# Optimization experiments

Measured on AMD Instinct MI355X. Metric: run time of the kernel, lower is better.

Reference implementation:

```python
import jax, jax.numpy as jnp
import numpy as np

B, S, HID = 1, 2048, 2048
NH = 32
NOPE, ROPE = 128, 64
QK = NOPE + ROPE
VD = 128
KV_RANK = 512
SW = 128            # sliding window (layer_types[layer_idx] == 'sliding_attention')
SCALE = QK ** -0.5
NEG = -1e9


def rotate_half(x):
    h = x.shape[-1] // 2
    return jnp.concatenate([-x[..., h:], x[..., :h]], axis=-1)


def setup_inputs() -> dict:
    key = jax.random.key(0)
    ks = jax.random.split(key, 8)

    def n(k, shape, s=0.02):
        return jax.random.normal(k, shape, dtype=jnp.float32) * s

    hidden = jax.random.normal(ks[0], (B, S, HID), dtype=jnp.float32)
    # HF-style RoPE tables, broadcast to [B, S, ROPE]
    pos = jnp.arange(S, dtype=jnp.float32)
    inv = 1.0 / (10000.0 ** (jnp.arange(0, ROPE, 2, dtype=jnp.float32) / ROPE))
    ang = pos[:, None] * inv[None, :]
    ang = jnp.concatenate([ang, ang], axis=-1)
    cos = jnp.broadcast_to(jnp.cos(ang)[None], (B, S, ROPE))
    sin = jnp.broadcast_to(jnp.sin(ang)[None], (B, S, ROPE))
    return dict(
        hidden_states=hidden, cos=cos, sin=sin,
        Wq=n(ks[1], (HID, NH * QK)), bq=jnp.zeros((NH * QK,), jnp.float32),
        Wkva=n(ks[2], (HID, KV_RANK + ROPE)), bkva=jnp.zeros((KV_RANK + ROPE,), jnp.float32),
        Wkvb=n(ks[3], (KV_RANK, NH * (NOPE + VD))),
        Wo=n(ks[4], (NH * VD, HID)), bo=jnp.zeros((HID,), jnp.float32),
        sinks=jax.random.normal(ks[5], (NH,), dtype=jnp.float32),
    )


def reference(hidden_states, cos, sin, Wq, bq, Wkva, bkva, Wkvb, Wo, bo, sinks):
    b, s = hidden_states.shape[:2]
    # Q projection -> [b, nh, s, qk_head_dim]
    q = (hidden_states @ Wq + bq).reshape(b, s, NH, QK).transpose(0, 2, 1, 3)
    q_nope, q_rope = q[..., :NOPE], q[..., NOPE:]
    # MLA: compressed KV latent + shared (MQA) rope key
    ckv = hidden_states @ Wkva + bkva                       # [b, s, rank+rope]
    kv_lat, k_rope = ckv[..., :KV_RANK], ckv[..., KV_RANK:]
    kv = (kv_lat @ Wkvb).reshape(b, s, NH, NOPE + VD).transpose(0, 2, 1, 3)
    k_nope, v = kv[..., :NOPE], kv[..., NOPE:]              # [b, nh, s, *]
    k_rope = k_rope.reshape(b, 1, s, ROPE)                  # mla_rope_num_kv_heads = 1
    # RoPE (HF apply_rotary_pos_emb, unsqueeze head dim)
    c, si = cos[:, None], sin[:, None]
    q_rope = q_rope * c + rotate_half(q_rope) * si
    k_rope = k_rope * c + rotate_half(k_rope) * si
    k_rope = jnp.broadcast_to(k_rope, (b, NH, s, ROPE))     # repeat_kv
    qs = jnp.concatenate([q_nope, q_rope], axis=-1)
    kk = jnp.concatenate([k_nope, k_rope], axis=-1)
    # attention logits with causal + sliding-window mask
    logits = jnp.einsum('bhqd,bhkd->bhqk', qs, kk) * SCALE
    i = jnp.arange(s)[:, None]
    j = jnp.arange(s)[None, :]
    allowed = (j <= i) & (i - j < SW)
    logits = jnp.where(allowed[None, None], logits, NEG)
    # sink-augmented softmax: append learned per-head sink logit, softmax, drop it
    sink = jnp.broadcast_to(sinks[None, :, None, None], (b, NH, s, 1))
    probs = jax.nn.softmax(jnp.concatenate([logits, sink], axis=-1), axis=-1)[..., :-1]
    out = jnp.einsum('bhqk,bhkd->bhqd', probs, v)           # [b, nh, s, vd]
    out = out.transpose(0, 2, 1, 3).reshape(b, s, NH * VD)
    return out @ Wo + bo
```

## Files before the change

kernel.cpp:

```cpp
#include <hip/hip_runtime.h>
#include <hip/hip_bf16.h>
#include <math.h>

#define S_LEN 2048
#define HID_DIM 2048
#define NH 32
#define NOPE 128
#define ROPE_D 64
#define QKD 192
#define VD 128
#define KV_RANK 512
#define SW 128
#define NQK (NH*QKD)
#define CKV_N (KV_RANK+ROPE_D)
#define KVN (NH*(NOPE+VD))
#define KNW (NH*NOPE)
#define OUT_HID 2048
#define ATT_SCALE 0.07216878364870323f
#define NEG_INF (-1e30f)

typedef __bf16 bf16x8 __attribute__((ext_vector_type(8)));
typedef float  f32x4  __attribute__((ext_vector_type(4)));

__device__ __forceinline__ void async_load16(const void* gp, void* lp) {
    __builtin_amdgcn_global_load_lds(
        (const __attribute__((address_space(1))) void*)gp,
        (__attribute__((address_space(3))) void*)lp, 16, 0, 0);
}

__global__ __launch_bounds__(256)
void prep(const float* __restrict__ hidden, __hip_bfloat16* __restrict__ hid_bf,
          const float* __restrict__ Wq,   __hip_bfloat16* __restrict__ WqT,
          const float* __restrict__ Wkva, __hip_bfloat16* __restrict__ WkvaT,
          const float* __restrict__ Wkvb, __hip_bfloat16* __restrict__ WkvbT,
          const float* __restrict__ Wo,   __hip_bfloat16* __restrict__ WoT)
{
    __shared__ float tile[64][65];
    int b = blockIdx.x;
    const int t = threadIdx.x;

    if (b < 4096) {
        int i = b * 256 + t;
        float4 v = ((const float4*)hidden)[i];
        hid_bf[i * 4 + 0] = __float2bfloat16(v.x);
        hid_bf[i * 4 + 1] = __float2bfloat16(v.y);
        hid_bf[i * 4 + 2] = __float2bfloat16(v.z);
        hid_bf[i * 4 + 3] = __float2bfloat16(v.w);
        return;
    }
    b -= 4096;
    const float* src; __hip_bfloat16* dst; int rows, cols, CX;
    if (b < 3072)                { src = Wq;   dst = WqT;   rows = 2048; cols = 6144; CX = 96;  }
    else if ((b -= 3072) < 288)  { src = Wkva; dst = WkvaT; rows = 2048; cols = 576;  CX = 9;   }
    else if ((b -= 288) < 1024)  { src = Wkvb; dst = WkvbT; rows = 512;  cols = 8192; CX = 128; }
    else { b -= 1024;              src = Wo;   dst = WoT;   rows = 4096; cols = 2048; CX = 32;  }

    const int bx = b % CX, by = b / CX;
    const int r0 = by * 64, c0 = bx * 64;

    {
        const int r  = t >> 4;
        const int c4 = (t & 15) * 4;
        #pragma unroll
        for (int i = 0; i < 4; ++i) {
            const int rr = r + i * 16;
            float4 v = *(const float4*)&src[(size_t)(r0 + rr) * cols + c0 + c4];
            tile[rr][c4 + 0] = v.x;
            tile[rr][c4 + 1] = v.y;
            tile[rr][c4 + 2] = v.z;
            tile[rr][c4 + 3] = v.w;
        }
    }
    __syncthreads();
    const int tx = t & 63, ty = t >> 6;
    #pragma unroll
    for (int i = 0; i < 16; ++i) {
        const int dr = ty + i * 4;
        dst[(size_t)(c0 + dr) * rows + r0 + tx] = __float2bfloat16(tile[tx][dr]);
    }
}

#define BAR()   __builtin_amdgcn_s_barrier()
#define LGKM0() asm volatile("s_waitcnt lgkmcnt(0)" ::: "memory")
#define VMC(n)  asm volatile("s_waitcnt vmcnt(" #n ")" ::: "memory")

__device__ __forceinline__ void gemm256_core(
    const __hip_bfloat16* __restrict__ A, int lda,
    const __hip_bfloat16* __restrict__ Bt, int ldbt,
    int m0, int n0, int kbeg, int nit,
    __hip_bfloat16* lds, f32x4 (&acc)[8][4])
{
    const int t = threadIdx.x;
    const int w = t >> 6, L = t & 63;
    const int lane15 = L & 15, quad = L >> 4;
    const int wr = w >> 2, wc = w & 3;

    const int prw = w * 8 + (L >> 3);
    const int c8  = ((L & 7) ^ ((L >> 3) & 7)) * 8;
    const __hip_bfloat16* gA = A  + (size_t)(m0 + prw) * lda  + kbeg + c8;
    const __hip_bfloat16* gB = Bt + (size_t)(n0 + prw) * ldbt + kbeg + c8;
    const int uA = w * 512;
    const int uB = 16384 + w * 512;

    const int cx0 = ((quad)     ^ (L & 7)) * 8;
    const int cx1 = ((4 + quad) ^ (L & 7)) * 8;
    const int ra  = wr * 8192 + lane15 * 64;
    const int rb  = 16384 + (wc >> 1) * 8192 + (wc & 1) * 4096 + lane15 * 64;

    bf16x8 af[4][2], bfr[4][2];

    auto STG_A = [&](int buf, int h, int kt) {
        const __hip_bfloat16* g = gA + (size_t)h * 128 * lda + kt * 64;
        __hip_bfloat16* lp = lds + buf * 32768 + h * 8192 + uA;
        async_load16(g, lp);
        async_load16(g + (size_t)64 * lda, lp + 4096);
    };
    auto STG_B = [&](int buf, int h, int kt) {
        const __hip_bfloat16* g = gB + (size_t)h * 128 * ldbt + kt * 64;
        __hip_bfloat16* lp = lds + buf * 32768 + h * 8192 + uB;
        async_load16(g, lp);
        async_load16(g + (size_t)64 * ldbt, lp + 4096);
    };
    auto LDA4 = [&](int buf, int mlo) {
        const __hip_bfloat16* p0 = lds + buf * 32768 + ra;
        #pragma unroll
        for (int j = 0; j < 4; ++j) {
            af[j][0] = *(const bf16x8*)(const void*)(p0 + (mlo + j) * 1024 + cx0);
            af[j][1] = *(const bf16x8*)(const void*)(p0 + (mlo + j) * 1024 + cx1);
        }
    };
    auto LDB2 = [&](int buf, int nlo) {
        const __hip_bfloat16* p0 = lds + buf * 32768 + rb;
        #pragma unroll
        for (int n = 0; n < 2; ++n) {
            bfr[nlo + n][0] = *(const bf16x8*)(const void*)(p0 + (nlo + n) * 1024 + cx0);
            bfr[nlo + n][1] = *(const bf16x8*)(const void*)(p0 + (nlo + n) * 1024 + cx1);
        }
    };
    auto MMQ = [&](int mlo, int nlo) {
        __builtin_amdgcn_s_setprio(1);
        #pragma unroll
        for (int j = 0; j < 4; ++j)
            #pragma unroll
            for (int n = 0; n < 2; ++n)
                #pragma unroll
                for (int ks = 0; ks < 2; ++ks)
                    acc[mlo + j][nlo + n] = __builtin_amdgcn_mfma_f32_16x16x32_bf16(
                        af[j][ks], bfr[nlo + n][ks], acc[mlo + j][nlo + n], 0, 0, 0);
        __builtin_amdgcn_s_setprio(0);
    };

    STG_A(0, 0, 0); STG_B(0, 0, 0); STG_B(0, 1, 0); STG_A(0, 1, 0);
    STG_A(1, 0, 1); STG_B(1, 0, 1); STG_B(1, 1, 1);
    VMC(6);
    BAR();

    for (int it = 0; it < nit; ++it) {
        const int t0 = 2 * it, t1 = t0 + 1;
        const bool nl = (it + 1 < nit);
        LDA4(0, 0); LDB2(0, 0); STG_A(1, 1, t1);
        BAR(); LGKM0(); MMQ(0, 0); BAR();
        LDB2(0, 2);
        BAR(); LGKM0(); MMQ(0, 2); BAR();
        LDA4(0, 4); if (nl) STG_B(0, 0, t0 + 2);
        BAR(); LGKM0(); MMQ(4, 2); BAR();
        if (nl) { STG_B(0, 1, t0 + 2); STG_A(0, 0, t0 + 2); }
        BAR(); MMQ(4, 0);
        if (nl) { VMC(6); } else { VMC(0); }
        BAR();
        LDA4(1, 0); LDB2(1, 0); if (nl) STG_A(0, 1, t0 + 2);
        BAR(); LGKM0(); MMQ(0, 0); BAR();
        LDB2(1, 2);
        BAR(); LGKM0(); MMQ(0, 2); BAR();
        LDA4(1, 4); if (nl) STG_B(1, 0, t1 + 2);
        BAR(); LGKM0(); MMQ(4, 2); BAR();
        if (nl) { STG_B(1, 1, t1 + 2); STG_A(1, 0, t1 + 2); }
        BAR(); MMQ(4, 0);
        if (nl) { VMC(6); }
        BAR();
    }
}

__global__ __launch_bounds__(512)
void gemm_q_ckv(const __hip_bfloat16* __restrict__ A,
                const __hip_bfloat16* __restrict__ BtQ,
                const __hip_bfloat16* __restrict__ BtKVA,
                const float* __restrict__ bq,
                const float* __restrict__ bkva,
                const float* __restrict__ cosb, const float* __restrict__ sinb,
                __hip_bfloat16* __restrict__ C,
                __hip_bfloat16* __restrict__ kvlat,
                __hip_bfloat16* __restrict__ kr)
{
    __shared__ __hip_bfloat16 lds[65536];
    const int bid = blockIdx.x;
    const bool is_q = (bid < 192);
    const int m0 = (is_q ? (bid / 24) : ((bid - 192) / 3)) * 256;
    const int n0 = (is_q ? (bid % 24) : ((bid - 192) % 3)) * 256;

    f32x4 acc[8][4];
    #pragma unroll
    for (int mi = 0; mi < 8; ++mi)
        #pragma unroll
        for (int ni = 0; ni < 4; ++ni) acc[mi][ni] = (f32x4){0.f, 0.f, 0.f, 0.f};

    gemm256_core(A, HID_DIM, is_q ? BtQ : BtKVA, HID_DIM, m0, n0, 0,
                 HID_DIM / 128, lds, acc);

    const int t = threadIdx.x;
    const int w = t >> 6, L = t & 63;
    const int lane15 = L & 15, quad = L >> 4;
    const int wr = w >> 2, wc = w & 3;
    const int ns = n0 + wc * 64;

    if (is_q) {
        const bool do_rope = ((ns % 192) == 128);
        float bv[4];
        #pragma unroll
        for (int ni = 0; ni < 4; ++ni) bv[ni] = bq[ns + ni * 16 + lane15];

        #pragma unroll
        for (int mi = 0; mi < 8; ++mi) {
            const int rbase = m0 + wr * 128 + mi * 16 + quad * 4;
            float vv[4][4];
            #pragma unroll
            for (int ni = 0; ni < 4; ++ni)
                #pragma unroll
                for (int p = 0; p < 4; ++p) vv[ni][p] = acc[mi][ni][p] + bv[ni];
            if (do_rope) {
                #pragma unroll
                for (int ni = 0; ni < 2; ++ni) {
                    const int dd = ni * 16 + lane15;
                    #pragma unroll
                    for (int p = 0; p < 4; ++p) {
                        const int srow = rbase + p;
                        const float c0 = cosb[srow * ROPE_D + dd];
                        const float c1 = cosb[srow * ROPE_D + dd + 32];
                        const float s0 = sinb[srow * ROPE_D + dd];
                        const float s1 = sinb[srow * ROPE_D + dd + 32];
                        const float x0 = vv[ni][p], x1 = vv[ni + 2][p];
                        vv[ni][p]     = x0 * c0 - x1 * s0;
                        vv[ni + 2][p] = x1 * c1 + x0 * s1;
                    }
                }
            }
            #pragma unroll
            for (int ni = 0; ni < 4; ++ni) {
                const int c = ns + ni * 16 + lane15;
                #pragma unroll
                for (int p = 0; p < 4; ++p)
                    C[(size_t)(rbase + p) * NQK + c] = __float2bfloat16(vv[ni][p] * ATT_SCALE);
            }
        }
    } else if (ns < KV_RANK) {
        float bv[4];
        #pragma unroll
        for (int ni = 0; ni < 4; ++ni) bv[ni] = bkva[ns + ni * 16 + lane15];
        #pragma unroll
        for (int mi = 0; mi < 8; ++mi) {
            const int s = m0 + wr * 128 + mi * 16 + quad * 4;
            #pragma unroll
            for (int ni = 0; ni < 4; ++ni) {
                const int c = ns + ni * 16 + lane15;
                #pragma unroll
                for (int p = 0; p < 4; ++p)
                    kvlat[(size_t)(s + p) * KV_RANK + c] =
                        __float2bfloat16(acc[mi][ni][p] + bv[ni]);
            }
        }
    } else if (ns == KV_RANK) {
        #pragma unroll
        for (int mi = 0; mi < 8; ++mi) {
            const int sb = m0 + wr * 128 + mi * 16 + quad * 4;
            #pragma unroll
            for (int ni = 0; ni < 2; ++ni) {
                const int d = ni * 16 + lane15;
                const float ba = bkva[512 + d], bb = bkva[544 + d];
                #pragma unroll
                for (int p = 0; p < 4; ++p) {
                    const int s = sb + p;
                    const float a = acc[mi][ni][p] + ba;
                    const float b = acc[mi][ni + 2][p] + bb;
                    const float c0 = cosb[s * ROPE_D + d], c1 = cosb[s * ROPE_D + d + 32];
                    const float s0 = sinb[s * ROPE_D + d], s1 = sinb[s * ROPE_D + d + 32];
                    kr[(size_t)s * ROPE_D + d]      = __float2bfloat16(a * c0 - b * s0);
                    kr[(size_t)s * ROPE_D + d + 32] = __float2bfloat16(b * c1 + a * s1);
                }
            }
        }
    }
}

__global__ __launch_bounds__(512)
void gemm_kv256(const __hip_bfloat16* __restrict__ A,
                const __hip_bfloat16* __restrict__ Bt,
                __hip_bfloat16* __restrict__ kn,
                __hip_bfloat16* __restrict__ vt)
{
    __shared__ __hip_bfloat16 lds[65536];
    const int m0 = blockIdx.y * 256, n0 = blockIdx.x * 256;
    f32x4 acc[8][4];
    #pragma unroll
    for (int mi = 0; mi < 8; ++mi)
        #pragma unroll
        for (int ni = 0; ni < 4; ++ni) acc[mi][ni] = (f32x4){0.f, 0.f, 0.f, 0.f};

    gemm256_core(A, KV_RANK, Bt, KV_RANK, m0, n0, 0, KV_RANK / 128, lds, acc);

    const int t = threadIdx.x;
    const int w = t >> 6, L = t & 63;
    const int lane15 = L & 15, quad = L >> 4;
    const int wr = w >> 2, wc = w & 3;
    const int ns = n0 + wc * 64;

    #pragma unroll
    for (int mi = 0; mi < 8; ++mi) {
        const int rbase = m0 + wr * 128 + mi * 16 + quad * 4;
        #pragma unroll
        for (int ni = 0; ni < 4; ++ni) {
            const int c = ns + ni * 16 + lane15;
            const int h = c >> 8, d = c & 255;
            if (d < NOPE) {
                #pragma unroll
                for (int p = 0; p < 4; ++p)
                    kn[(size_t)(rbase + p) * KNW + h * NOPE + d] = __float2bfloat16(acc[mi][ni][p]);
            } else {
                ushort4 pk;
                __hip_bfloat16 b0 = __float2bfloat16(acc[mi][ni][0]);
                __hip_bfloat16 b1 = __float2bfloat16(acc[mi][ni][1]);
                __hip_bfloat16 b2 = __float2bfloat16(acc[mi][ni][2]);
                __hip_bfloat16 b3 = __float2bfloat16(acc[mi][ni][3]);
                pk.x = *(unsigned short*)&b0; pk.y = *(unsigned short*)&b1;
                pk.z = *(unsigned short*)&b2; pk.w = *(unsigned short*)&b3;
                *(ushort4*)(vt + (size_t)(h * VD + (d - NOPE)) * S_LEN + rbase) = pk;
            }
        }
    }
}

__global__ __launch_bounds__(512)
void gemm_partial256(const __hip_bfloat16* __restrict__ A, int lda,
                     const __hip_bfloat16* __restrict__ Bt, int ldbt,
                     float* __restrict__ P, int ldp, size_t zstride, int KL)
{
    __shared__ __hip_bfloat16 lds[65536];
    const int m0 = blockIdx.y * 256, n0 = blockIdx.x * 256;
    const int z  = blockIdx.z;
    f32x4 acc[8][4];
    #pragma unroll
    for (int mi = 0; mi < 8; ++mi)
        #pragma unroll
        for (int ni = 0; ni < 4; ++ni) acc[mi][ni] = (f32x4){0.f, 0.f, 0.f, 0.f};

    gemm256_core(A, lda, Bt, ldbt, m0, n0, z * KL, KL / 128, lds, acc);

    const int t = threadIdx.x;
    const int w = t >> 6, L = t & 63;
    const int lane15 = L & 15, quad = L >> 4;
    const int wr = w >> 2, wc = w & 3;
    float* Pz = P + (size_t)z * zstride;

    #pragma unroll
    for (int mi = 0; mi < 8; ++mi) {
        const int rbase = m0 + wr * 128 + mi * 16 + quad * 4;
        #pragma unroll
        for (int ni = 0; ni < 4; ++ni) {
            const int c = n0 + wc * 64 + ni * 16 + lane15;
            #pragma unroll
            for (int p = 0; p < 4; ++p)
                Pz[(size_t)(rbase + p) * ldp + c] = acc[mi][ni][p];
        }
    }
}

__global__ __launch_bounds__(256)
void wo_reduce4(const float* __restrict__ P, const float* __restrict__ bo,
                float* __restrict__ out)
{
    const size_t i = (size_t)blockIdx.x * 256 + threadIdx.x;
    const size_t zs = (size_t)S_LEN * OUT_HID;
    float4 a = ((const float4*)P)[i];
    float4 b = ((const float4*)(P + zs))[i];
    float4 c = ((const float4*)(P + 2 * zs))[i];
    float4 d = ((const float4*)(P + 3 * zs))[i];
    const int col = (int)((i * 4) & (OUT_HID - 1));
    float4 bb = *(const float4*)(bo + col);
    float4 o;
    o.x = a.x + b.x + c.x + d.x + bb.x;
    o.y = a.y + b.y + c.y + d.y + bb.y;
    o.z = a.z + b.z + c.z + d.z + bb.z;
    o.w = a.w + b.w + c.w + d.w + bb.w;
    ((float4*)out)[i] = o;
}

#define SS 170
#define SP 168
#define KSTR 200
#define VSTR 40

__global__ __launch_bounds__(256)
void attn_mfma2(const __hip_bfloat16* __restrict__ q,
                const __hip_bfloat16* __restrict__ kn,
                const __hip_bfloat16* __restrict__ kr,
                const __hip_bfloat16* __restrict__ vt,
                const float* __restrict__ sinks,
                __hip_bfloat16* __restrict__ out)
{
    __shared__ float lds_s[32 * SS];
    __shared__ __hip_bfloat16 lds_p[32 * SP];
    __shared__ __hip_bfloat16 lds_kv[32 * KSTR];

    const int h  = blockIdx.y;
    const int q0 = blockIdx.x * 32;
    const int t  = threadIdx.x;
    const int w  = t >> 6;
    const int L  = t & 63;
    const int lane15 = L & 15, quad = L >> 4;
    const int wm = (w & 1) * 16;
    const int wn = (w >> 1) * 16;

    int lo = q0 - SW + 1; if (lo < 0) lo = 0;
    const int cb = lo & ~31;
    const int nc = ((q0 - cb) >> 5) + 1;

    bf16x8 qf[6];
    {
        const __hip_bfloat16* qrow = q + (size_t)(q0 + wm + lane15) * NQK + h * QKD;
        #pragma unroll
        for (int kk = 0; kk < 6; ++kk)
            qf[kk] = *(const bf16x8*)(const void*)(qrow + kk * 32 + quad * 8);
    }

    for (int cc = 0; cc < nc; ++cc) {
        const int c0 = cb + cc * 32;
        __syncthreads();
        #pragma unroll
        for (int e = t; e < 768; e += 256) {
            const int row = e / 24, slot = e % 24;
            const int j = c0 + row;
            const __hip_bfloat16* g = (slot < 16)
                ? kn + (size_t)j * KNW + h * NOPE + slot * 8
                : kr + (size_t)j * ROPE_D + (slot - 16) * 8;
            *(bf16x8*)(void*)(lds_kv + row * KSTR + slot * 8) = *(const bf16x8*)(const void*)g;
        }
        __syncthreads();

        f32x4 s = (f32x4){0.f, 0.f, 0.f, 0.f};
        #pragma unroll
        for (int kk = 0; kk < 6; ++kk) {
            bf16x8 bf = *(const bf16x8*)(const void*)(lds_kv + (wn + lane15) * KSTR + kk * 32 + quad * 8);
            s = __builtin_amdgcn_mfma_f32_16x16x32_bf16(qf[kk], bf, s, 0, 0, 0);
        }
        const int j = c0 + wn + lane15;
        #pragma unroll
        for (int p = 0; p < 4; ++p) {
            const int i = q0 + wm + quad * 4 + p;
            const bool ok = (j <= i) && (i - j < SW);
            lds_s[(wm + quad * 4 + p) * SS + cc * 32 + wn + lane15] = ok ? s[p] : NEG_INF;
        }
    }
    __syncthreads();

    {
        const int r = t >> 3, g = t & 7;
        const int ncols = nc * 32;
        const float sink = sinks[h];
        float mx = sink;
        for (int c = g; c < ncols; c += 8)
            mx = fmaxf(mx, lds_s[r * SS + c]);
        #pragma unroll
        for (int off = 1; off < 8; off <<= 1)
            mx = fmaxf(mx, __shfl_xor(mx, off));
        float sum = 0.f;
        for (int c = g; c < ncols; c += 8) {
            float e = __expf(lds_s[r * SS + c] - mx);
            lds_s[r * SS + c] = e;
            sum += e;
        }
        #pragma unroll
        for (int off = 1; off < 8; off <<= 1)
            sum += __shfl_xor(sum, off);
        const float inv = 1.0f / (sum + __expf(sink - mx));
        for (int c = g; c < ncols; c += 8)
            lds_p[r * SP + c] = __float2bfloat16(lds_s[r * SS + c] * inv);
    }

    f32x4 oacc[4];
    #pragma unroll
    for (int ni = 0; ni < 4; ++ni) oacc[ni] = (f32x4){0.f, 0.f, 0.f, 0.f};

    for (int cc = 0; cc < nc; ++cc) {
        const int c0 = cb + cc * 32;
        __syncthreads();
        #pragma unroll
        for (int e = t; e < 512; e += 256) {
            const int row = e >> 2, slot = e & 3;
            *(bf16x8*)(void*)(lds_kv + row * VSTR + slot * 8) =
                *(const bf16x8*)(const void*)(vt + (size_t)(h * VD + row) * S_LEN + c0 + slot * 8);
        }
        __syncthreads();

        bf16x8 ap = *(const bf16x8*)(const void*)(lds_p + (wm + lane15) * SP + cc * 32 + quad * 8);
        #pragma unroll
        for (int ni = 0; ni < 4; ++ni) {
            bf16x8 bv = *(const bf16x8*)(const void*)(lds_kv + ((w >> 1) * 64 + ni * 16 + lane15) * VSTR + quad * 8);
            oacc[ni] = __builtin_amdgcn_mfma_f32_16x16x32_bf16(ap, bv, oacc[ni], 0, 0, 0);
        }
    }

    #pragma unroll
    for (int ni = 0; ni < 4; ++ni) {
        const int col = h * VD + (w >> 1) * 64 + ni * 16 + lane15;
        #pragma unroll
        for (int p = 0; p < 4; ++p) {
            const int row = q0 + wm + quad * 4 + p;
            out[(size_t)row * (NH * VD) + col] = __float2bfloat16(oacc[ni][p]);
        }
    }
}

extern "C" void kernel_launch(void* const* d_in, const int* in_sizes, int n_in,
                              void* d_out, int out_size, void* d_ws, size_t ws_size,
                              hipStream_t stream) {
    const float* hidden = (const float*)d_in[0];
    const float* cosb   = (const float*)d_in[1];
    const float* sinb   = (const float*)d_in[2];
    const float* Wq     = (const float*)d_in[3];
    const float* bq     = (const float*)d_in[4];
    const float* Wkva   = (const float*)d_in[5];
    const float* bkva   = (const float*)d_in[6];
    const float* Wkvb   = (const float*)d_in[7];
    const float* Wo     = (const float*)d_in[8];
    const float* bo     = (const float*)d_in[9];
    const float* sinks  = (const float*)d_in[10];
    float* out = (float*)d_out;

    uint8_t* p = (uint8_t*)d_ws;
    __hip_bfloat16* attn_bf = (__hip_bfloat16*)p; p += (size_t)S_LEN * NH * VD * 2;
    __hip_bfloat16* WoT     = (__hip_bfloat16*)p; p += (size_t)OUT_HID * (NH*VD) * 2;
    __hip_bfloat16* q_bf    = (__hip_bfloat16*)p; p += (size_t)S_LEN * NQK * 2;
    __hip_bfloat16* hid_bf  = (__hip_bfloat16*)p; p += (size_t)S_LEN * HID_DIM * 2;
    __hip_bfloat16* WqT     = (__hip_bfloat16*)p; p += (size_t)NQK * HID_DIM * 2;
    __hip_bfloat16* WkvaT   = (__hip_bfloat16*)p; p += (size_t)640 * HID_DIM * 2;
    __hip_bfloat16* WkvbT   = (__hip_bfloat16*)p; p += (size_t)KVN * KV_RANK * 2;
    __hip_bfloat16* kn_bf   = (__hip_bfloat16*)p; p += (size_t)S_LEN * KNW * 2;
    __hip_bfloat16* vt_bf   = (__hip_bfloat16*)p; p += (size_t)S_LEN * NH * VD * 2;
    __hip_bfloat16* kr_bf   = (__hip_bfloat16*)p; p += (size_t)S_LEN * ROPE_D * 2;
    __hip_bfloat16* kvlat   = (__hip_bfloat16*)p; p += (size_t)S_LEN * KV_RANK * 2;
    float* WoP = (float*)q_bf;

    prep<<<10528, 256, 0, stream>>>(hidden, hid_bf, Wq, WqT, Wkva, WkvaT,
                                    Wkvb, WkvbT, Wo, WoT);

    gemm_q_ckv<<<216, 512, 0, stream>>>(
        hid_bf, WqT, WkvaT, bq, bkva, cosb, sinb, q_bf, kvlat, kr_bf);

    gemm_kv256<<<dim3(KVN / 256, S_LEN / 256), 512, 0, stream>>>(
        kvlat, WkvbT, kn_bf, vt_bf);

    attn_mfma2<<<dim3(S_LEN / 32, NH), 256, 0, stream>>>(
        q_bf, kn_bf, kr_bf, vt_bf, sinks, attn_bf);

    gemm_partial256<<<dim3(OUT_HID / 256, S_LEN / 256, 4), 512, 0, stream>>>(
        attn_bf, NH * VD, WoT, NH * VD, WoP, OUT_HID, (size_t)S_LEN * OUT_HID, 1024);

    wo_reduce4<<<(S_LEN * OUT_HID / 4) / 256, 256, 0, stream>>>(WoP, bo, out);
}
```

Measured before the change: 357.2 us.

## Overlap Wkvb/Wo weight transposes with Q/CKV GEMM using extra blocks

Moves the bf16 transpose of Wkvb and Wo out of the prep kernel and into 40 extra workgroups appended to the Q/CKV GEMM launch, so that conversion work fills CUs left idle by the 216 GEMM blocks on a 256-CU device. It also reorders the GEMM main loop so the vmcnt wait happens before the barrier that precedes the final MMA quarter, which merges two barrier regions. The extra blocks share the launch's large LDS and 512-thread configuration. Their grid-stride loop may extend the GEMM kernel's tail if the transposes take longer than the GEMM.

Result: slower. 376.9 us (+5.5%).

```diff
diff --git a/kernel.cpp b/kernel.cpp
--- a/kernel.cpp
+++ b/kernel.cpp
@@ -31,9 +31,7 @@
 __global__ __launch_bounds__(256)
 void prep(const float* __restrict__ hidden, __hip_bfloat16* __restrict__ hid_bf,
           const float* __restrict__ Wq,   __hip_bfloat16* __restrict__ WqT,
-          const float* __restrict__ Wkva, __hip_bfloat16* __restrict__ WkvaT,
-          const float* __restrict__ Wkvb, __hip_bfloat16* __restrict__ WkvbT,
-          const float* __restrict__ Wo,   __hip_bfloat16* __restrict__ WoT)
+          const float* __restrict__ Wkva, __hip_bfloat16* __restrict__ WkvaT)
 {
     __shared__ float tile[64][65];
     int b = blockIdx.x;
@@ -50,10 +48,8 @@
     }
     b -= 4096;
     const float* src; __hip_bfloat16* dst; int rows, cols, CX;
-    if (b < 3072)                { src = Wq;   dst = WqT;   rows = 2048; cols = 6144; CX = 96;  }
-    else if ((b -= 3072) < 288)  { src = Wkva; dst = WkvaT; rows = 2048; cols = 576;  CX = 9;   }
-    else if ((b -= 288) < 1024)  { src = Wkvb; dst = WkvbT; rows = 512;  cols = 8192; CX = 128; }
-    else { b -= 1024;              src = Wo;   dst = WoT;   rows = 4096; cols = 2048; CX = 32;  }
+    if (b < 3072) { src = Wq;   dst = WqT;   rows = 2048; cols = 6144; CX = 96; }
+    else { b -= 3072; src = Wkva; dst = WkvaT; rows = 2048; cols = 576;  CX = 9;  }
 
     const int bx = b % CX, by = b / CX;
     const int r0 = by * 64, c0 = bx * 64;
@@ -164,20 +160,17 @@
         BAR(); LGKM0(); MMQ(0, 2); BAR();
         LDA4(0, 4); if (nl) STG_B(0, 0, t0 + 2);
         BAR(); LGKM0(); MMQ(4, 2); BAR();
-        if (nl) { STG_B(0, 1, t0 + 2); STG_A(0, 0, t0 + 2); }
-        BAR(); MMQ(4, 0);
-        if (nl) { VMC(6); } else { VMC(0); }
-        BAR();
+        if (nl) { STG_B(0, 1, t0 + 2); STG_A(0, 0, t0 + 2); VMC(6); }
+        else    { VMC(0); }
+        BAR(); MMQ(4, 0); BAR();
         LDA4(1, 0); LDB2(1, 0); if (nl) STG_A(0, 1, t0 + 2);
         BAR(); LGKM0(); MMQ(0, 0); BAR();
         LDB2(1, 2);
         BAR(); LGKM0(); MMQ(0, 2); BAR();
         LDA4(1, 4); if (nl) STG_B(1, 0, t1 + 2);
         BAR(); LGKM0(); MMQ(4, 2); BAR();
-        if (nl) { STG_B(1, 1, t1 + 2); STG_A(1, 0, t1 + 2); }
-        BAR(); MMQ(4, 0);
-        if (nl) { VMC(6); }
-        BAR();
+        if (nl) { STG_B(1, 1, t1 + 2); STG_A(1, 0, t1 + 2); VMC(6); }
+        BAR(); MMQ(4, 0); BAR();
     }
 }
 
@@ -190,10 +183,45 @@
                 const float* __restrict__ cosb, const float* __restrict__ sinb,
                 __hip_bfloat16* __restrict__ C,
                 __hip_bfloat16* __restrict__ kvlat,
-                __hip_bfloat16* __restrict__ kr)
+                __hip_bfloat16* __restrict__ kr,
+                const float* __restrict__ Wkvb, __hip_bfloat16* __restrict__ WkvbT,
+                const float* __restrict__ Wo,   __hip_bfloat16* __restrict__ WoT)
 {
     __shared__ __hip_bfloat16 lds[65536];
     const int bid = blockIdx.x;
+    const int t = threadIdx.x;
+
+    if (bid >= 216) {
+        float (*tile)[65] = (float (*)[65])(void*)lds;
+        const int r  = t >> 4;
+        const int c4 = (t & 15) * 4;
+        const int tx = t & 63, ty = t >> 6;
+        for (int id = bid - 216; id < 3072; id += 40) {
+            const float* src; __hip_bfloat16* dst; int rows, cols, CX, tid;
+            if (id < 1024) { src = Wkvb; dst = WkvbT; rows = 512;  cols = 8192; CX = 128; tid = id; }
+            else           { src = Wo;   dst = WoT;   rows = 4096; cols = 2048; CX = 32;  tid = id - 1024; }
+            const int bx = tid % CX, by = tid / CX;
+            const int r0 = by * 64, c0 = bx * 64;
+            #pragma unroll
+            for (int i = 0; i < 2; ++i) {
+                const int rr = r + i * 32;
+                float4 v = *(const float4*)&src[(size_t)(r0 + rr) * cols + c0 + c4];
+                tile[rr][c4 + 0] = v.x;
+                tile[rr][c4 + 1] = v.y;
+                tile[rr][c4 + 2] = v.z;
+                tile[rr][c4 + 3] = v.w;
+            }
+            __syncthreads();
+            #pragma unroll
+            for (int i = 0; i < 8; ++i) {
+                const int dr = ty + i * 8;
+                dst[(size_t)(c0 + dr) * rows + r0 + tx] = __float2bfloat16(tile[tx][dr]);
+            }
+            __syncthreads();
+        }
+        return;
+    }
+
     const bool is_q = (bid < 192);
     const int m0 = (is_q ? (bid / 24) : ((bid - 192) / 3)) * 256;
     const int n0 = (is_q ? (bid % 24) : ((bid - 192) % 3)) * 256;
@@ -207,7 +235,6 @@
     gemm256_core(A, HID_DIM, is_q ? BtQ : BtKVA, HID_DIM, m0, n0, 0,
                  HID_DIM / 128, lds, acc);
 
-    const int t = threadIdx.x;
     const int w = t >> 6, L = t & 63;
     const int lane15 = L & 15, quad = L >> 4;
     const int wr = w >> 2, wc = w & 3;
@@ -549,11 +576,11 @@
     __hip_bfloat16* kvlat   = (__hip_bfloat16*)p; p += (size_t)S_LEN * KV_RANK * 2;
     float* WoP = (float*)q_bf;
 
-    prep<<<10528, 256, 0, stream>>>(hidden, hid_bf, Wq, WqT, Wkva, WkvaT,
-                                    Wkvb, WkvbT, Wo, WoT);
-
-    gemm_q_ckv<<<216, 512, 0, stream>>>(
-        hid_bf, WqT, WkvaT, bq, bkva, cosb, sinb, q_bf, kvlat, kr_bf);
+    prep<<<7456, 256, 0, stream>>>(hidden, hid_bf, Wq, WqT, Wkva, WkvaT);
+
+    gemm_q_ckv<<<256, 512, 0, stream>>>(
+        hid_bf, WqT, WkvaT, bq, bkva, cosb, sinb, q_bf, kvlat, kr_bf,
+        Wkvb, WkvbT, Wo, WoT);
 
     gemm_kv256<<<dim3(KVN / 256, S_LEN / 256), 512, 0, stream>>>(
         kvlat, WkvbT, kn_bf, vt_bf);
```
